# Kernel optimization log

Hardware: AMD Instinct MI355X
Metric: run time of the kernel (lower is better)

## Reference

```python
import jax, jax.numpy as jnp
import numpy as np

S = 4096
V = 50000
E = 512
H = 512
CE = 128
CH = 128
T = 50


def _lstm_dir(x, W_ih, W_hh, b, reverse):
    # x: [S, D]; PyTorch gate order i, f, g, o. b = b_ih + b_hh fused.
    gx = x @ W_ih.T + b  # [S, 4H] precomputed input contribution
    Hd = W_hh.shape[1]
    def step(carry, g_t):
        h, c = carry
        g = g_t + h @ W_hh.T
        i, f, gg, o = jnp.split(g, 4, axis=-1)
        c = jax.nn.sigmoid(f) * c + jax.nn.sigmoid(i) * jnp.tanh(gg)
        h = jax.nn.sigmoid(o) * jnp.tanh(c)
        return (h, c), h
    init = (jnp.zeros((Hd,), x.dtype), jnp.zeros((Hd,), x.dtype))
    _, hs = jax.lax.scan(step, init, gx, reverse=reverse)
    return hs  # [S, H]


def _bilstm(x, Wih_f, Whh_f, b_f, Wih_b, Whh_b, b_b):
    fwd = _lstm_dir(x, Wih_f, Whh_f, b_f, False)
    bwd = _lstm_dir(x, Wih_b, Whh_b, b_b, True)
    return jnp.concatenate([fwd, bwd], axis=-1)  # [S, 2H]


def _viterbi(emissions, start_t, end_t, trans):
    # emissions: [S, T]. Standard CRF Viterbi (torchcrf semantics).
    score0 = start_t + emissions[0]  # [T]
    def step(score, emit):
        m = score[:, None] + trans          # [T_prev, T_cur]
        bp = jnp.argmax(m, axis=0)          # best previous tag for each cur tag
        new_score = jnp.max(m, axis=0) + emit
        return new_score, bp
    final, bps = jax.lax.scan(step, score0, emissions[1:])  # bps: [S-1, T]
    final = final + end_t
    last = jnp.argmax(final)
    def back(tag, bp):
        prev = bp[tag]
        return prev, prev
    _, path_head = jax.lax.scan(back, last, bps, reverse=True)  # [S-1]
    return jnp.concatenate([path_head, last[None]])  # [S]


def setup_inputs() -> dict:
    key = jax.random.key(0)
    ks = jax.random.split(key, 20)
    s = 0.05
    inp = {
        'sentence': jax.random.randint(ks[0], (S,), 0, V),
        'char_sentence': jax.random.randint(ks[1], (S,), 0, V),
        'word_emb': jax.random.normal(ks[2], (V, E), jnp.float32) * s,
        'char_emb': jax.random.normal(ks[3], (V, CE), jnp.float32) * s,
        # char BiLSTM
        'cWih_f': jax.random.normal(ks[4], (4 * CH, CE), jnp.float32) * s,
        'cWhh_f': jax.random.normal(ks[5], (4 * CH, CH), jnp.float32) * s,
        'cb_f': jnp.zeros((4 * CH,), jnp.float32),
        'cWih_b': jax.random.normal(ks[6], (4 * CH, CE), jnp.float32) * s,
        'cWhh_b': jax.random.normal(ks[7], (4 * CH, CH), jnp.float32) * s,
        'cb_b': jnp.zeros((4 * CH,), jnp.float32),
        # word BiLSTM (input dim E + 2*CH)
        'wWih_f': jax.random.normal(ks[8], (4 * H, E + 2 * CH), jnp.float32) * s,
        'wWhh_f': jax.random.normal(ks[9], (4 * H, H), jnp.float32) * s,
        'wb_f': jnp.zeros((4 * H,), jnp.float32),
        'wWih_b': jax.random.normal(ks[10], (4 * H, E + 2 * CH), jnp.float32) * s,
        'wWhh_b': jax.random.normal(ks[11], (4 * H, H), jnp.float32) * s,
        'wb_b': jnp.zeros((4 * H,), jnp.float32),
        # hidden2tag
        'W_tag': jax.random.normal(ks[12], (T, 2 * H), jnp.float32) * s,
        'b_tag': jnp.zeros((T,), jnp.float32),
        # CRF params
        'start_t': jax.random.normal(ks[13], (T,), jnp.float32) * s,
        'end_t': jax.random.normal(ks[14], (T,), jnp.float32) * s,
        'trans': jax.random.normal(ks[15], (T, T), jnp.float32) * s,
    }
    return inp


def reference(sentence, char_sentence, word_emb, char_emb,
              cWih_f, cWhh_f, cb_f, cWih_b, cWhh_b, cb_b,
              wWih_f, wWhh_f, wb_f, wWih_b, wWhh_b, wb_b,
              W_tag, b_tag, start_t, end_t, trans):
    we = word_emb[sentence]          # [S, E]
    ce = char_emb[char_sentence]     # [S, CE]
    char_out = _bilstm(ce, cWih_f, cWhh_f, cb_f, cWih_b, cWhh_b, cb_b)  # [S, 2*CH]
    emb = jnp.concatenate([we, char_out], axis=-1)  # [S, E + 2*CH]
    lstm_out = _bilstm(emb, wWih_f, wWhh_f, wb_f, wWih_b, wWhh_b, wb_b)  # [S, 2H]
    tag_space = lstm_out @ W_tag.T + b_tag  # [S, T] emissions
    path = _viterbi(tag_space, start_t, end_t, trans)  # [S] int32 tags
    return path
```

## Files before the change

### kernel.cpp

```cpp
#include <hip/hip_runtime.h>
#include <math.h>

#define SQ   4096
#define EDIM 512
#define CEDIM 128
#define CHH  128
#define WH   512
#define NT   50

typedef unsigned long long ull;

__device__ __forceinline__ float sigf(float x) { return 1.0f / (1.0f + expf(-x)); }

#define PIN4(V) asm volatile("" : "+v"(V.x), "+v"(V.y), "+v"(V.z), "+v"(V.w));

__device__ __forceinline__ void ld8x_sc0(const ull* p, ull& q0, ull& q1, ull& q2,
                                         ull& q3, ull& q4, ull& q5, ull& q6, ull& q7) {
    asm volatile("global_load_dwordx2 %0, %8, off sc0\n\t"
                 "global_load_dwordx2 %1, %8, off offset:8 sc0\n\t"
                 "global_load_dwordx2 %2, %8, off offset:16 sc0\n\t"
                 "global_load_dwordx2 %3, %8, off offset:24 sc0\n\t"
                 "global_load_dwordx2 %4, %8, off offset:32 sc0\n\t"
                 "global_load_dwordx2 %5, %8, off offset:40 sc0\n\t"
                 "global_load_dwordx2 %6, %8, off offset:48 sc0\n\t"
                 "global_load_dwordx2 %7, %8, off offset:56 sc0\n\t"
                 "s_waitcnt vmcnt(0)"
                 : "=&v"(q0), "=&v"(q1), "=&v"(q2), "=&v"(q3),
                   "=&v"(q4), "=&v"(q5), "=&v"(q6), "=&v"(q7)
                 : "v"(p) : "memory");
}
__device__ __forceinline__ ull ld_mir(const ull* p) {
    return __hip_atomic_load(p, __ATOMIC_RELAXED, __HIP_MEMORY_SCOPE_AGENT);
}
__device__ __forceinline__ void st_plain8(ull* p, ull v) {
    asm volatile("global_store_dwordx2 %0, %1, off" :: "v"(p), "v"(v) : "memory");
}
__device__ __forceinline__ void st_mir(ull* p, ull v) {
    __hip_atomic_store(p, v, __ATOMIC_RELAXED, __HIP_MEMORY_SCOPE_AGENT);
}
__device__ __forceinline__ unsigned umin2(unsigned a, unsigned b) { return a < b ? a : b; }

#define FMA4(W, off) { float4 h4 = *(const float4*)&hc[off]; \
    a0 += W.x * h4.x; a1 += W.y * h4.y; a2 += W.z * h4.z; a3 += W.w * h4.w; }

__global__ __launch_bounds__(256) void k1_gather_cgx(
    const int* __restrict__ sent, const int* __restrict__ csent,
    const float* __restrict__ wemb, const float* __restrict__ cemb,
    const float* __restrict__ cWih_f, const float* __restrict__ cb_f,
    const float* __restrict__ cWih_b, const float* __restrict__ cb_b,
    float* __restrict__ we_g, float* __restrict__ cgx)
{
    const int tid = threadIdx.x;
    const int t0 = blockIdx.x * 16;
    __shared__ __align__(16) float ceL[16][128];
    __shared__ int sids[16], cids[16];
    if (tid < 16) sids[tid] = sent[t0 + tid];
    else if (tid < 32) cids[tid - 16] = csent[t0 + tid - 16];
    __syncthreads();
    {
        int f4 = tid;
        for (int q = 0; q < 2; ++q, f4 += 256) {
            int r = f4 >> 5, k4 = f4 & 31;
            float4 v = *(const float4*)&cemb[(size_t)cids[r] * CEDIM + k4 * 4];
            *(float4*)&ceL[r][k4 * 4] = v;
        }
    }
    {
        int f4 = tid;
        for (int q = 0; q < 8; ++q, f4 += 256) {
            int r = f4 >> 7, k4 = f4 & 127;
            float4 v = *(const float4*)&wemb[(size_t)sids[r] * EDIM + k4 * 4];
            *(float4*)&we_g[(size_t)(t0 + r) * EDIM + k4 * 4] = v;
        }
    }
    __syncthreads();
    for (int q = 0; q < 4; ++q) {
        int j = q * 256 + tid;
        int d = j >> 9, r = j & 511;
        const float* Wih = d ? cWih_b : cWih_f;
        const float* cb = d ? cb_b : cb_f;
        float b = cb[r];
        float acc[16];
#pragma unroll
        for (int tt = 0; tt < 16; ++tt) acc[tt] = b;
        for (int k4 = 0; k4 < 32; ++k4) {
            float4 wv = *(const float4*)&Wih[r * CEDIM + k4 * 4];
#pragma unroll
            for (int tt = 0; tt < 16; ++tt) {
                acc[tt] += wv.x * ceL[tt][k4 * 4 + 0] + wv.y * ceL[tt][k4 * 4 + 1]
                         + wv.z * ceL[tt][k4 * 4 + 2] + wv.w * ceL[tt][k4 * 4 + 3];
            }
        }
#pragma unroll
        for (int tt = 0; tt < 16; ++tt)
            cgx[((size_t)d * SQ + (t0 + tt)) * 512 + r] = acc[tt];
    }
}

__global__ __launch_bounds__(1024, 4) void k2_charlstm_gemm(
    const float* __restrict__ cWhh_f, const float* __restrict__ cWhh_b,
    const float* __restrict__ cgx, float* __restrict__ cho,
    const float* __restrict__ we_g,
    const float* __restrict__ wWih_f, const float* __restrict__ wb_f,
    const float* __restrict__ wWih_b, const float* __restrict__ wb_b,
    float* __restrict__ wgx)
{
    const int tid = threadIdx.x;
    __shared__ __align__(16) float At[32][68];
    __shared__ __align__(16) float Bt[32][128];
    __shared__ __align__(16) float hstC[128];
    __shared__ float partC[2][516];

    if (blockIdx.x < 2) {
        const int dir = blockIdx.x;
        const float* Whh = dir ? cWhh_b : cWhh_f;
        const int row = tid & 511;
        const int half = tid >> 9;
        const float4* wp = (const float4*)&Whh[(size_t)row * CHH + half * 64];
        float4 w0 = wp[0], w1 = wp[1], w2 = wp[2], w3 = wp[3];
        float4 w4 = wp[4], w5 = wp[5], w6 = wp[6], w7 = wp[7];
        float4 w8 = wp[8], w9 = wp[9], w10 = wp[10], w11 = wp[11];
        float4 w12 = wp[12], w13 = wp[13], w14 = wp[14], w15 = wp[15];
        PIN4(w0) PIN4(w1) PIN4(w2) PIN4(w3) PIN4(w4) PIN4(w5) PIN4(w6) PIN4(w7)
        PIN4(w8) PIN4(w9) PIN4(w10) PIN4(w11) PIN4(w12) PIN4(w13) PIN4(w14) PIN4(w15)

        const float* gxc = cgx + (size_t)dir * SQ * 512;
        float cst = 0.f;
        float gxp0 = 0.f, gxp1 = 0.f;
        if (tid < 512) {
            gxp0 = gxc[(size_t)(dir ? (SQ - 1) : 0) * 512 + tid];
            gxp1 = gxc[(size_t)(dir ? (SQ - 2) : 1) * 512 + tid];
        }
        if (tid < 32) *(float4*)&hstC[tid * 4] = make_float4(0, 0, 0, 0);
        __syncthreads();
        for (int t = 0; t < SQ; ++t) {
            const int x = dir ? (SQ - 1 - t) : t;
            float gxv = gxp0;
            gxp0 = gxp1;
            if (tid < 512 && t + 2 < SQ) {
                const int x2 = dir ? (SQ - 3 - t) : (t + 2);
                gxp1 = gxc[(size_t)x2 * 512 + tid];
            }
            float a0 = 0.f, a1 = 0.f, a2 = 0.f, a3 = 0.f;
            const float* hc = &hstC[half * 64];
            FMA4(w0, 0)   FMA4(w1, 4)   FMA4(w2, 8)   FMA4(w3, 12)
            FMA4(w4, 16)  FMA4(w5, 20)  FMA4(w6, 24)  FMA4(w7, 28)
            FMA4(w8, 32)  FMA4(w9, 36)  FMA4(w10, 40) FMA4(w11, 44)
            FMA4(w12, 48) FMA4(w13, 52) FMA4(w14, 56) FMA4(w15, 60)
            float dot = (a0 + a1) + (a2 + a3);
            partC[half][row] = half ? dot : (dot + gxv);
            __syncthreads();
            if (tid < 128) {
                float siv = partC[0][tid]       + partC[1][tid];
                float sfv = partC[0][128 + tid] + partC[1][128 + tid];
                float sgv = partC[0][256 + tid] + partC[1][256 + tid];
                float sov = partC[0][384 + tid] + partC[1][384 + tid];
                float iv = sigf(siv), fv = sigf(sfv), ov = sigf(sov);
                float yg = sigf(sgv + sgv);
                float gv = yg + yg - 1.f;
                cst = fv * cst + iv * gv;
                float ts = sigf(cst + cst);
                float h = ov * (ts + ts - 1.f);
                hstC[tid] = h;
                cho[(size_t)x * 256 + dir * CHH + tid] = h;
            }
            __syncthreads();
        }
        return;
    }
    const int tile = blockIdx.x - 2;
    const int dir = tile >> 10;
    const int rem = tile & 1023;
    const int mb = rem >> 4;
    const int nb = rem & 15;
    const float* Wih = dir ? wWih_b : wWih_f;
    const float* wb = dir ? wb_b : wb_f;
    float* C = wgx + (size_t)dir * SQ * 2048;
    const int tm = tid >> 6, tn = tid & 63;
    float acc[4][2];
#pragma unroll
    for (int i = 0; i < 4; ++i) { acc[i][0] = 0.f; acc[i][1] = 0.f; }
    for (int kb = 0; kb < 16; ++kb) {
        if (tid < 512) {
            int rowm = tid >> 3, k4 = tid & 7;
            float4 v = *(const float4*)&we_g[(size_t)(mb * 64 + rowm) * EDIM + kb * 32 + k4 * 4];
            At[k4 * 4 + 0][rowm] = v.x; At[k4 * 4 + 1][rowm] = v.y;
            At[k4 * 4 + 2][rowm] = v.z; At[k4 * 4 + 3][rowm] = v.w;
        }
        {
            int rr = tid >> 3, k4 = tid & 7;
            float4 v = *(const float4*)&Wih[(size_t)(nb * 128 + rr) * 768 + kb * 32 + k4 * 4];
            Bt[k4 * 4 + 0][rr] = v.x; Bt[k4 * 4 + 1][rr] = v.y;
            Bt[k4 * 4 + 2][rr] = v.z; Bt[k4 * 4 + 3][rr] = v.w;
        }
        __syncthreads();
#pragma unroll
        for (int kk = 0; kk < 32; ++kk) {
            float4 a4 = *(const float4*)&At[kk][tm * 4];
            float2 b2 = *(const float2*)&Bt[kk][tn * 2];
            acc[0][0] += a4.x * b2.x; acc[0][1] += a4.x * b2.y;
            acc[1][0] += a4.y * b2.x; acc[1][1] += a4.y * b2.y;
            acc[2][0] += a4.z * b2.x; acc[2][1] += a4.z * b2.y;
            acc[3][0] += a4.w * b2.x; acc[3][1] += a4.w * b2.y;
        }
        __syncthreads();
    }
    float2 wbv = *(const float2*)&wb[nb * 128 + tn * 2];
#pragma unroll
    for (int i = 0; i < 4; ++i) {
        float2 o;
        o.x = acc[i][0] + wbv.x; o.y = acc[i][1] + wbv.y;
        *(float2*)&C[(size_t)(mb * 64 + tm * 4 + i) * 2048 + nb * 128 + tn * 2] = o;
    }
}

__global__ __launch_bounds__(512, 2) void k3_gemm_char(
    const float* __restrict__ cho,
    const float* __restrict__ wWih_f, const float* __restrict__ wWih_b,
    float* __restrict__ wgx)
{
    const int tid = threadIdx.x;
    const int tile = blockIdx.x;
    const int dir = tile >> 10;
    const int rem = tile & 1023;
    const int mb = rem >> 4, nb = rem & 15;
    const float* Wih = dir ? wWih_b : wWih_f;
    float* C = wgx + (size_t)dir * SQ * 2048;
    __shared__ __align__(16) float At[32][68];
    __shared__ __align__(16) float Bt[32][128];
    const int tm = tid >> 5, tn = tid & 31;
    float acc[4][4];
#pragma unroll
    for (int i = 0; i < 4; ++i)
#pragma unroll
        for (int jj = 0; jj < 4; ++jj) acc[i][jj] = 0.f;
    for (int kb = 0; kb < 8; ++kb) {
        {
            int rowm = tid >> 3, k4 = tid & 7;
            float4 v = *(const float4*)&cho[(size_t)(mb * 64 + rowm) * 256 + kb * 32 + k4 * 4];
            At[k4 * 4 + 0][rowm] = v.x; At[k4 * 4 + 1][rowm] = v.y;
            At[k4 * 4 + 2][rowm] = v.z; At[k4 * 4 + 3][rowm] = v.w;
        }
#pragma unroll
        for (int q = 0; q < 2; ++q) {
            int f4 = q * 512 + tid;
            int rr = f4 >> 3, k4 = f4 & 7;
            float4 v = *(const float4*)&Wih[(size_t)(nb * 128 + rr) * 768 + 512 + kb * 32 + k4 * 4];
            Bt[k4 * 4 + 0][rr] = v.x; Bt[k4 * 4 + 1][rr] = v.y;
            Bt[k4 * 4 + 2][rr] = v.z; Bt[k4 * 4 + 3][rr] = v.w;
        }
        __syncthreads();
#pragma unroll
        for (int kk = 0; kk < 32; ++kk) {
            float4 a4 = *(const float4*)&At[kk][tm * 4];
            float4 b4 = *(const float4*)&Bt[kk][tn * 4];
            acc[0][0] += a4.x * b4.x; acc[0][1] += a4.x * b4.y; acc[0][2] += a4.x * b4.z; acc[0][3] += a4.x * b4.w;
            acc[1][0] += a4.y * b4.x; acc[1][1] += a4.y * b4.y; acc[1][2] += a4.y * b4.z; acc[1][3] += a4.y * b4.w;
            acc[2][0] += a4.z * b4.x; acc[2][1] += a4.z * b4.y; acc[2][2] += a4.z * b4.z; acc[2][3] += a4.z * b4.w;
            acc[3][0] += a4.w * b4.x; acc[3][1] += a4.w * b4.y; acc[3][2] += a4.w * b4.z; acc[3][3] += a4.w * b4.w;
        }
        __syncthreads();
    }
#pragma unroll
    for (int i = 0; i < 4; ++i) {
        float* cp = &C[(size_t)(mb * 64 + tm * 4 + i) * 2048 + nb * 128 + tn * 4];
        float4 o = *(float4*)cp;
        o.x += acc[i][0]; o.y += acc[i][1]; o.z += acc[i][2]; o.w += acc[i][3];
        *(float4*)cp = o;
    }
}

__global__ __launch_bounds__(1024, 4) void k4_word_lstm(
    const float* __restrict__ wWhh_f, const float* __restrict__ wWhh_b,
    const float* __restrict__ wgx, float* __restrict__ lstm, ull* __restrict__ pairs)
{
    const int res = blockIdx.x & 7;
    if (res > 1) return;
    const int dir = res;
    const int wid = blockIdx.x >> 3;
    const int tid = threadIdx.x;
    const int k = tid >> 6;
    const int r = tid & 63;
    const int g = r >> 4, u = r & 15;
    const float* Whh = dir ? wWhh_b : wWhh_f;
    const int G = g * WH + wid * 16 + u;
    const float4* wp = (const float4*)&Whh[(size_t)G * WH + k * 32];
    float4 w0 = wp[0], w1 = wp[1], w2 = wp[2], w3 = wp[3];
    float4 w4 = wp[4], w5 = wp[5], w6 = wp[6], w7 = wp[7];
    PIN4(w0) PIN4(w1) PIN4(w2) PIN4(w3) PIN4(w4) PIN4(w5) PIN4(w6) PIN4(w7)

    __shared__ __align__(16) float hst[512];
    __shared__ float part[16][65];

    ull* wpf = pairs;
    ull* wpm = pairs + 2048;
    const float* gx = wgx + (size_t)dir * SQ * 2048;
    float cst = 0.f;
    int useFast = 1, alive = 1;
    for (int t = 0; t < SQ; ++t) {
        const int x = dir ? (SQ - 1 - t) : t;
        float gxv = 0.f;
        if (tid < 64)
            gxv = gx[(size_t)x * 2048 + (size_t)(tid >> 4) * 512 + wid * 16 + (tid & 15)];
        if (t == 0) {
            if (tid < 128) *(float4*)&hst[tid * 4] = make_float4(0, 0, 0, 0);
        } else if (tid < 64) {
            const size_t boff = ((size_t)((t - 1) & 1) * 2 + dir) * 512 + tid * 8;
            const ull* pf = wpf + boff;
            const ull* pm = wpm + boff;
            ull q0 = 0, q1 = 0, q2 = 0, q3 = 0, q4 = 0, q5 = 0, q6 = 0, q7 = 0;
            int spins = 0;
            while (alive) {
                if (useFast) {
                    ld8x_sc0(pf, q0, q1, q2, q3, q4, q5, q6, q7);
                } else {
                    q0 = ld_mir(pm + 0); q1 = ld_mir(pm + 1);
                    q2 = ld_mir(pm + 2); q3 = ld_mir(pm + 3);
                    q4 = ld_mir(pm + 4); q5 = ld_mir(pm + 5);
                    q6 = ld_mir(pm + 6); q7 = ld_mir(pm + 7);
                }
                unsigned tm = umin2(umin2(umin2((unsigned)(q0 >> 32), (unsigned)(q1 >> 32)),
                                          umin2((unsigned)(q2 >> 32), (unsigned)(q3 >> 32))),
                                    umin2(umin2((unsigned)(q4 >> 32), (unsigned)(q5 >> 32)),
                                          umin2((unsigned)(q6 >> 32), (unsigned)(q7 >> 32))));
                if (__all(tm >= (unsigned)t)) break;
                ++spins;
                if (useFast && spins > 2048) { useFast = 0; spins = 0; }
                if (!useFast && spins > (1 << 20)) alive = 0;
                __builtin_amdgcn_s_sleep(1);
            }
            float* hd = &hst[tid * 8];
            hd[0] = __uint_as_float((unsigned)q0); hd[1] = __uint_as_float((unsigned)q1);
            hd[2] = __uint_as_float((unsigned)q2); hd[3] = __uint_as_float((unsigned)q3);
            hd[4] = __uint_as_float((unsigned)q4); hd[5] = __uint_as_float((unsigned)q5);
            hd[6] = __uint_as_float((unsigned)q6); hd[7] = __uint_as_float((unsigned)q7);
        }
        __syncthreads();
        float a0 = 0.f, a1 = 0.f, a2 = 0.f, a3 = 0.f;
        const float* hc = &hst[k * 32];
        FMA4(w0, 0)  FMA4(w1, 4)  FMA4(w2, 8)  FMA4(w3, 12)
        FMA4(w4, 16) FMA4(w5, 20) FMA4(w6, 24) FMA4(w7, 28)
        part[k][r] = (a0 + a1) + (a2 + a3);
        __syncthreads();
        if (tid < 64) {
            float s = gxv;
#pragma unroll
            for (int kk = 0; kk < 16; ++kk) s += part[kk][tid];
            const bool isg = ((tid >> 4) == 2);
            float y = sigf(isg ? (s + s) : s);
            float val = isg ? (y + y - 1.f) : y;
            float fv = __shfl(val, 16 + (tid & 15));
            float gv = __shfl(val, 32 + (tid & 15));
            float ov = __shfl(val, 48 + (tid & 15));
            if (tid < 16) {
                cst = fv * cst + val * gv;
                float ts = sigf(cst + cst);
                float h = ov * (ts + ts - 1.f);
                const int unit = wid * 16 + tid;
                lstm[(size_t)x * 1024 + dir * WH + unit] = h;
                ull q = ((ull)(unsigned)(t + 1) << 32) | (ull)__float_as_uint(h);
                const size_t poff = ((size_t)(t & 1) * 2 + dir) * 512 + unit;
                st_plain8(wpf + poff, q);
                st_mir(wpm + poff, q);
            }
        }
    }
}

__global__ __launch_bounds__(64) void k5_emis(
    const float* __restrict__ lstm, const float* __restrict__ Wtag,
    const float* __restrict__ btag, float* __restrict__ emis)
{
    const int t = blockIdx.x, tid = threadIdx.x;
    __shared__ __align__(16) float rowL[1024];
#pragma unroll
    for (int q = 0; q < 4; ++q) {
        int f4 = q * 64 + tid;
        *(float4*)&rowL[f4 * 4] = *(const float4*)&lstm[(size_t)t * 1024 + f4 * 4];
    }
    __syncthreads();
    if (tid < NT) {
        float a0 = 0.f, a1 = 0.f, a2 = 0.f, a3 = 0.f;
        const float* wr = Wtag + (size_t)tid * 1024;
        for (int k4 = 0; k4 < 256; ++k4) {
            float4 wv = *(const float4*)&wr[k4 * 4];
            a0 += wv.x * rowL[k4 * 4 + 0];
            a1 += wv.y * rowL[k4 * 4 + 1];
            a2 += wv.z * rowL[k4 * 4 + 2];
            a3 += wv.w * rowL[k4 * 4 + 3];
        }
        emis[(size_t)t * NT + tid] = btag[tid] + (a0 + a1) + (a2 + a3);
    }
}

__global__ __launch_bounds__(256) void k6a_viterbi(
    const float* __restrict__ emis, const float* __restrict__ start_t,
    const float* __restrict__ end_t, const float* __restrict__ trans,
    unsigned char* __restrict__ bpb, int* __restrict__ last)
{
    const int tid = threadIdx.x;
    const int g = tid >> 6, c = tid & 63;
    __shared__ float sc[64];
    __shared__ float pbest[4][64];
    __shared__ int pbp[4][64];
    const int p0 = g * 13;
    float tr[13];
#pragma unroll
    for (int i = 0; i < 13; ++i) {
        int p = p0 + i;
        tr[i] = (c < NT && p < NT) ? trans[p * NT + c] : -1e30f;
    }
    if (tid < 64) sc[tid] = (tid < NT) ? (start_t[tid] + emis[tid]) : -1e30f;
    __syncthreads();
    for (int t = 1; t < SQ; ++t) {
        float best = -1e30f; int bp = 0;
#pragma unroll
        for (int i = 0; i < 13; ++i) {
            float v = sc[p0 + i] + tr[i];
            if (v > best) { best = v; bp = p0 + i; }
        }
        pbest[g][c] = best; pbp[g][c] = bp;
        __syncthreads();
        if (tid < NT) {
            float b = pbest[0][tid]; int bb = pbp[0][tid];
#pragma unroll
            for (int gg = 1; gg < 4; ++gg) {
                float v = pbest[gg][tid];
                if (v > b) { b = v; bb = pbp[gg][tid]; }
            }
            bpb[(size_t)t * NT + tid] = (unsigned char)bb;
            sc[tid] = b + emis[(size_t)t * NT + tid];
        }
        __syncthreads();
    }
    if (tid == 0) {
        float b = -1e30f; int bi = 0;
        for (int cc = 0; cc < NT; ++cc) {
            float v = sc[cc] + end_t[cc];
            if (v > b) { b = v; bi = cc; }
        }
        *last = bi;
    }
}

__global__ __launch_bounds__(64) void k6b_maps(
    const unsigned char* __restrict__ bpb, int* __restrict__ map_)
{
    const int k = blockIdx.x;
    const int e = threadIdx.x;
    if (k == 0 || e >= NT) return;
    int tag = e;
    for (int i = 63; i >= 0; --i) {
        int t = k * 64 + i;
        tag = bpb[(size_t)t * NT + tag];
    }
    map_[k * NT + e] = tag;
}

__global__ __launch_bounds__(64) void k6c_backtrack(
    const unsigned char* __restrict__ bpb, const int* __restrict__ map_,
    const int* __restrict__ last, int* __restrict__ path)
{
    __shared__ int B[64];
    if (threadIdx.x == 0) {
        int tag = *last;
        B[63] = tag;
        for (int k = 63; k >= 1; --k) {
            tag = map_[k * NT + tag];
            B[k - 1] = tag;
        }
    }
    __syncthreads();
    const int k = threadIdx.x;
    int tag = B[k];
    for (int i = 63; i >= 0; --i) {
        int t = k * 64 + i;
        path[t] = tag;
        if (t >= 1) tag = bpb[(size_t)t * NT + tag];
    }
}

extern "C" void kernel_launch(void* const* d_in, const int* in_sizes, int n_in,
                              void* d_out, int out_size, void* d_ws, size_t ws_size,
                              hipStream_t stream)
{
    const int* sent = (const int*)d_in[0];
    const int* csent = (const int*)d_in[1];
    const float* wemb = (const float*)d_in[2];
    const float* cemb = (const float*)d_in[3];
    const float* cWih_f = (const float*)d_in[4];
    const float* cWhh_f = (const float*)d_in[5];
    const float* cb_f = (const float*)d_in[6];
    const float* cWih_b = (const float*)d_in[7];
    const float* cWhh_b = (const float*)d_in[8];
    const float* cb_b = (const float*)d_in[9];
    const float* wWih_f = (const float*)d_in[10];
    const float* wWhh_f = (const float*)d_in[11];
    const float* wb_f = (const float*)d_in[12];
    const float* wWih_b = (const float*)d_in[13];
    const float* wWhh_b = (const float*)d_in[14];
    const float* wb_b = (const float*)d_in[15];
    const float* Wtag = (const float*)d_in[16];
    const float* btag = (const float*)d_in[17];
    const float* start_t = (const float*)d_in[18];
    const float* end_t = (const float*)d_in[19];
    const float* trans = (const float*)d_in[20];
    int* path = (int*)d_out;

    float* ws = (float*)d_ws;
    float* we_g = ws;
    float* cgx  = we_g + (size_t)SQ * EDIM;
    float* cho  = cgx + (size_t)2 * SQ * 512;
    float* wgx  = cho + (size_t)SQ * 256;
    float* lstm = wgx + (size_t)2 * SQ * 2048;
    float* emis = lstm + (size_t)SQ * 1024;
    ull* pairs  = (ull*)(emis + (size_t)SQ * NT);
    int* map_   = (int*)(pairs + 5120);
    int* lastp  = map_ + 64 * NT;
    unsigned char* bpb = (unsigned char*)(lastp + 4);

    (void)hipMemsetAsync(pairs, 0, 5120 * sizeof(ull), stream);

    k1_gather_cgx<<<SQ / 16, 256, 0, stream>>>(sent, csent, wemb, cemb,
                                               cWih_f, cb_f, cWih_b, cb_b, we_g, cgx);
    k2_charlstm_gemm<<<2 + 2048, 1024, 0, stream>>>(cWhh_f, cWhh_b, cgx, cho, we_g,
                                                    wWih_f, wb_f, wWih_b, wb_b, wgx);
    k3_gemm_char<<<2048, 512, 0, stream>>>(cho, wWih_f, wWih_b, wgx);
    k4_word_lstm<<<256, 1024, 0, stream>>>(wWhh_f, wWhh_b, wgx, lstm, pairs);
    k5_emis<<<SQ, 64, 0, stream>>>(lstm, Wtag, btag, emis);
    k6a_viterbi<<<1, 256, 0, stream>>>(emis, start_t, end_t, trans, bpb, lastp);
    k6b_maps<<<64, 64, 0, stream>>>(bpb, map_);
    k6c_backtrack<<<1, 64, 0, stream>>>(bpb, map_, lastp, path);
}
```

Before: 14.66 ms.

## Halve char-LSTM block to 512 threads with full-row register weights

The char BiLSTM recurrence now runs with 512 threads per block, each holding a full 128-wide W_hh row in registers (32 float4), instead of 1024 threads splitting each row in halves. This removes the partial-sum combine through shared memory and makes the per-step barriers cheaper, at the cost of twice the FMA chain length per thread and higher register pressure. The co-scheduled GEMM tiles in the same kernel are adjusted to 512 threads with a 4x4 per-thread micro-tile.

```diff
diff --git a/kernel.cpp b/kernel.cpp
--- a/kernel.cpp
+++ b/kernel.cpp
@@ -43,6 +43,8 @@
 #define FMA4(W, off) { float4 h4 = *(const float4*)&hc[off]; \
     a0 += W.x * h4.x; a1 += W.y * h4.y; a2 += W.z * h4.z; a3 += W.w * h4.w; }
 
+#define CW(n) float4 w##n = wp[n]; PIN4(w##n)
+
 __global__ __launch_bounds__(256) void k1_gather_cgx(
     const int* __restrict__ sent, const int* __restrict__ csent,
     const float* __restrict__ wemb, const float* __restrict__ cemb,
@@ -97,7 +99,7 @@
     }
 }
 
-__global__ __launch_bounds__(1024, 4) void k2_charlstm_gemm(
+__global__ __launch_bounds__(512, 2) void k2_charlstm_gemm(
     const float* __restrict__ cWhh_f, const float* __restrict__ cWhh_b,
     const float* __restrict__ cgx, float* __restrict__ cho,
     const float* __restrict__ we_g,
@@ -109,52 +111,47 @@
     __shared__ __align__(16) float At[32][68];
     __shared__ __align__(16) float Bt[32][128];
     __shared__ __align__(16) float hstC[128];
-    __shared__ float partC[2][516];
+    __shared__ float gb[512];
 
     if (blockIdx.x < 2) {
         const int dir = blockIdx.x;
         const float* Whh = dir ? cWhh_b : cWhh_f;
-        const int row = tid & 511;
-        const int half = tid >> 9;
-        const float4* wp = (const float4*)&Whh[(size_t)row * CHH + half * 64];
-        float4 w0 = wp[0], w1 = wp[1], w2 = wp[2], w3 = wp[3];
-        float4 w4 = wp[4], w5 = wp[5], w6 = wp[6], w7 = wp[7];
-        float4 w8 = wp[8], w9 = wp[9], w10 = wp[10], w11 = wp[11];
-        float4 w12 = wp[12], w13 = wp[13], w14 = wp[14], w15 = wp[15];
-        PIN4(w0) PIN4(w1) PIN4(w2) PIN4(w3) PIN4(w4) PIN4(w5) PIN4(w6) PIN4(w7)
-        PIN4(w8) PIN4(w9) PIN4(w10) PIN4(w11) PIN4(w12) PIN4(w13) PIN4(w14) PIN4(w15)
+        const int row = tid;
+        const float4* wp = (const float4*)&Whh[(size_t)row * CHH];
+        CW(0)  CW(1)  CW(2)  CW(3)  CW(4)  CW(5)  CW(6)  CW(7)
+        CW(8)  CW(9)  CW(10) CW(11) CW(12) CW(13) CW(14) CW(15)
+        CW(16) CW(17) CW(18) CW(19) CW(20) CW(21) CW(22) CW(23)
+        CW(24) CW(25) CW(26) CW(27) CW(28) CW(29) CW(30) CW(31)
 
         const float* gxc = cgx + (size_t)dir * SQ * 512;
         float cst = 0.f;
-        float gxp0 = 0.f, gxp1 = 0.f;
-        if (tid < 512) {
-            gxp0 = gxc[(size_t)(dir ? (SQ - 1) : 0) * 512 + tid];
-            gxp1 = gxc[(size_t)(dir ? (SQ - 2) : 1) * 512 + tid];
-        }
+        float gxp0 = gxc[(size_t)(dir ? (SQ - 1) : 0) * 512 + row];
+        float gxp1 = gxc[(size_t)(dir ? (SQ - 2) : 1) * 512 + row];
         if (tid < 32) *(float4*)&hstC[tid * 4] = make_float4(0, 0, 0, 0);
         __syncthreads();
         for (int t = 0; t < SQ; ++t) {
             const int x = dir ? (SQ - 1 - t) : t;
             float gxv = gxp0;
             gxp0 = gxp1;
-            if (tid < 512 && t + 2 < SQ) {
+            if (t + 2 < SQ) {
                 const int x2 = dir ? (SQ - 3 - t) : (t + 2);
-                gxp1 = gxc[(size_t)x2 * 512 + tid];
+                gxp1 = gxc[(size_t)x2 * 512 + row];
             }
             float a0 = 0.f, a1 = 0.f, a2 = 0.f, a3 = 0.f;
-            const float* hc = &hstC[half * 64];
-            FMA4(w0, 0)   FMA4(w1, 4)   FMA4(w2, 8)   FMA4(w3, 12)
-            FMA4(w4, 16)  FMA4(w5, 20)  FMA4(w6, 24)  FMA4(w7, 28)
-            FMA4(w8, 32)  FMA4(w9, 36)  FMA4(w10, 40) FMA4(w11, 44)
-            FMA4(w12, 48) FMA4(w13, 52) FMA4(w14, 56) FMA4(w15, 60)
-            float dot = (a0 + a1) + (a2 + a3);
-            partC[half][row] = half ? dot : (dot + gxv);
+            const float* hc = hstC;
+            FMA4(w0, 0)    FMA4(w1, 4)    FMA4(w2, 8)    FMA4(w3, 12)
+            FMA4(w4, 16)   FMA4(w5, 20)   FMA4(w6, 24)   FMA4(w7, 28)
+            FMA4(w8, 32)   FMA4(w9, 36)   FMA4(w10, 40)  FMA4(w11, 44)
+            FMA4(w12, 48)  FMA4(w13, 52)  FMA4(w14, 56)  FMA4(w15, 60)
+            FMA4(w16, 64)  FMA4(w17, 68)  FMA4(w18, 72)  FMA4(w19, 76)
+            FMA4(w20, 80)  FMA4(w21, 84)  FMA4(w22, 88)  FMA4(w23, 92)
+            FMA4(w24, 96)  FMA4(w25, 100) FMA4(w26, 104) FMA4(w27, 108)
+            FMA4(w28, 112) FMA4(w29, 116) FMA4(w30, 120) FMA4(w31, 124)
+            gb[row] = (a0 + a1) + (a2 + a3) + gxv;
             __syncthreads();
             if (tid < 128) {
-                float siv = partC[0][tid]       + partC[1][tid];
-                float sfv = partC[0][128 + tid] + partC[1][128 + tid];
-                float sgv = partC[0][256 + tid] + partC[1][256 + tid];
-                float sov = partC[0][384 + tid] + partC[1][384 + tid];
+                float siv = gb[tid], sfv = gb[128 + tid];
+                float sgv = gb[256 + tid], sov = gb[384 + tid];
                 float iv = sigf(siv), fv = sigf(sfv), ov = sigf(sov);
                 float yg = sigf(sgv + sgv);
                 float gv = yg + yg - 1.f;
@@ -176,19 +173,23 @@
     const float* Wih = dir ? wWih_b : wWih_f;
     const float* wb = dir ? wb_b : wb_f;
     float* C = wgx + (size_t)dir * SQ * 2048;
-    const int tm = tid >> 6, tn = tid & 63;
-    float acc[4][2];
-#pragma unroll
-    for (int i = 0; i < 4; ++i) { acc[i][0] = 0.f; acc[i][1] = 0.f; }
+    const int tm = tid >> 5, tn = tid & 31;
+    float acc[4][4];
+#pragma unroll
+    for (int i = 0; i < 4; ++i)
+#pragma unroll
+        for (int jj = 0; jj < 4; ++jj) acc[i][jj] = 0.f;
     for (int kb = 0; kb < 16; ++kb) {
-        if (tid < 512) {
+        {
             int rowm = tid >> 3, k4 = tid & 7;
             float4 v = *(const float4*)&we_g[(size_t)(mb * 64 + rowm) * EDIM + kb * 32 + k4 * 4];
             At[k4 * 4 + 0][rowm] = v.x; At[k4 * 4 + 1][rowm] = v.y;
             At[k4 * 4 + 2][rowm] = v.z; At[k4 * 4 + 3][rowm] = v.w;
         }
-        {
-            int rr = tid >> 3, k4 = tid & 7;
+#pragma unroll
+        for (int q = 0; q < 2; ++q) {
+            int f4 = q * 512 + tid;
+            int rr = f4 >> 3, k4 = f4 & 7;
             float4 v = *(const float4*)&Wih[(size_t)(nb * 128 + rr) * 768 + kb * 32 + k4 * 4];
             Bt[k4 * 4 + 0][rr] = v.x; Bt[k4 * 4 + 1][rr] = v.y;
             Bt[k4 * 4 + 2][rr] = v.z; Bt[k4 * 4 + 3][rr] = v.w;
@@ -197,20 +198,21 @@
 #pragma unroll
         for (int kk = 0; kk < 32; ++kk) {
             float4 a4 = *(const float4*)&At[kk][tm * 4];
-            float2 b2 = *(const float2*)&Bt[kk][tn * 2];
-            acc[0][0] += a4.x * b2.x; acc[0][1] += a4.x * b2.y;
-            acc[1][0] += a4.y * b2.x; acc[1][1] += a4.y * b2.y;
-            acc[2][0] += a4.z * b2.x; acc[2][1] += a4.z * b2.y;
-            acc[3][0] += a4.w * b2.x; acc[3][1] += a4.w * b2.y;
-        }
-        __syncthreads();
-    }
-    float2 wbv = *(const float2*)&wb[nb * 128 + tn * 2];
+            float4 b4 = *(const float4*)&Bt[kk][tn * 4];
+            acc[0][0] += a4.x * b4.x; acc[0][1] += a4.x * b4.y; acc[0][2] += a4.x * b4.z; acc[0][3] += a4.x * b4.w;
+            acc[1][0] += a4.y * b4.x; acc[1][1] += a4.y * b4.y; acc[1][2] += a4.y * b4.z; acc[1][3] += a4.y * b4.w;
+            acc[2][0] += a4.z * b4.x; acc[2][1] += a4.z * b4.y; acc[2][2] += a4.z * b4.z; acc[2][3] += a4.z * b4.w;
+            acc[3][0] += a4.w * b4.x; acc[3][1] += a4.w * b4.y; acc[3][2] += a4.w * b4.z; acc[3][3] += a4.w * b4.w;
+        }
+        __syncthreads();
+    }
+    float4 wbv = *(const float4*)&wb[nb * 128 + tn * 4];
 #pragma unroll
     for (int i = 0; i < 4; ++i) {
-        float2 o;
+        float4 o;
         o.x = acc[i][0] + wbv.x; o.y = acc[i][1] + wbv.y;
-        *(float2*)&C[(size_t)(mb * 64 + tm * 4 + i) * 2048 + nb * 128 + tn * 2] = o;
+        o.z = acc[i][2] + wbv.z; o.w = acc[i][3] + wbv.w;
+        *(float4*)&C[(size_t)(mb * 64 + tm * 4 + i) * 2048 + nb * 128 + tn * 4] = o;
     }
 }
 
@@ -523,8 +525,8 @@
 
     k1_gather_cgx<<<SQ / 16, 256, 0, stream>>>(sent, csent, wemb, cemb,
                                                cWih_f, cb_f, cWih_b, cb_b, we_g, cgx);
-    k2_charlstm_gemm<<<2 + 2048, 1024, 0, stream>>>(cWhh_f, cWhh_b, cgx, cho, we_g,
-                                                    wWih_f, wb_f, wWih_b, wb_b, wgx);
+    k2_charlstm_gemm<<<2 + 2048, 512, 0, stream>>>(cWhh_f, cWhh_b, cgx, cho, we_g,
+                                                   wWih_f, wb_f, wWih_b, wb_b, wgx);
     k3_gemm_char<<<2048, 512, 0, stream>>>(cho, wWih_f, wWih_b, wgx);
     k4_word_lstm<<<256, 1024, 0, stream>>>(wWhh_f, wWhh_b, wgx, lstm, pairs);
     k5_emis<<<SQ, 64, 0, stream>>>(lstm, Wtag, btag, emis);
```

After: 16.61 ms. +13.3%, slower.
